# Performance work log

Hardware: AMD Instinct MI355X
Metric: run time of the kernel (lower is better)

The kernel has to match this reference:

```python
import jax, jax.numpy as jnp
import numpy as np

N = 200000      # number of nodes / samples
D = 256         # embedding_dim
K = 20          # n_clusters


def setup_inputs() -> dict:
    key = jax.random.key(0)
    k1, k2 = jax.random.split(key)
    embeddings = jax.random.normal(k1, (N, D), dtype=jnp.float32)
    # indicator P has orthonormal-ish columns in the original (top-k eigenvectors
    # of ZZ^T); random values are fine for a correctness baseline of the math.
    indicator = jax.random.normal(k2, (N, K), dtype=jnp.float32)
    return {"embeddings": embeddings, "indicator": indicator}


def reference(embeddings, indicator):
    # Jc = tr(Z Z^T) - tr(P^T Z Z^T P)
    # tr(Z Z^T) = sum(Z * Z)
    term1 = jnp.sum(embeddings * embeddings)
    # tr(P^T Z Z^T P) = || Z^T P ||_F^2 ; Z^T P is [D, K] (tiny), avoids N x N gram.
    ztp = jnp.einsum('nd,nk->dk', embeddings, indicator)
    term2 = jnp.sum(ztp * ztp)
    return term1 - term2
```

## Files before the change

kernel.cpp:

```cpp
#include <hip/hip_runtime.h>

#define NN 200000
#define DD 256
#define KK 20
#define CHUNK 200
#define NB (NN / CHUNK)
#define RPW (CHUNK / 4)
#define DEPTH 8


typedef __attribute__((address_space(3))) unsigned int lds_uint;
typedef const __attribute__((address_space(1))) unsigned int glb_uint;
#define DMA(gp, lp) \
  __builtin_amdgcn_global_load_lds((glb_uint*)(gp), (lds_uint*)(lp), 16, 0, 0)
#define WAITVM(N) asm volatile("s_waitcnt vmcnt(" #N ")" ::: "memory")

#define SCOMP(i, zv)                                                        \
  {                                                                         \
    const float4* pr_ = (const float4*)(pl + (((i) * 4 + w) * KK));         \
    float4 p0_ = pr_[0], p1_ = pr_[1], p2_ = pr_[2], p3_ = pr_[3],          \
           p4_ = pr_[4];                                                    \
    float zz_[4] = {zv.x, zv.y, zv.z, zv.w};                                \
    float pv_[KK] = {p0_.x, p0_.y, p0_.z, p0_.w, p1_.x, p1_.y, p1_.z,       \
                     p1_.w, p2_.x, p2_.y, p2_.z, p2_.w, p3_.x, p3_.y,       \
                     p3_.z, p3_.w, p4_.x, p4_.y, p4_.z, p4_.w};             \
    t1 += zz_[0] * zz_[0] + zz_[1] * zz_[1];                                \
    t1 += zz_[2] * zz_[2] + zz_[3] * zz_[3];                                \
    _Pragma("unroll") for (int k_ = 0; k_ < KK; ++k_) {                     \
      _Pragma("unroll") for (int c_ = 0; c_ < 4; ++c_)                      \
          acc[k_][c_] += zz_[c_] * pv_[k_];                                 \
    }                                                                       \
  }

#define TAIL(S, N)                                                          \
  {                                                                         \
    WAITVM(N);                                                              \
    float4 z = ((const float4*)(myring + ((S) & (DEPTH - 1)) * DD))[lane];  \
    SCOMP(S, z);                                                            \
  }

__global__ __launch_bounds__(256)
__attribute__((amdgpu_waves_per_eu(3, 3))) void egac_main(
    const float* __restrict__ Z, const float* __restrict__ P,
    float* __restrict__ ztp_part, float* __restrict__ t1_part) {
  __shared__ float ring[4 * DEPTH * DD];
  __shared__ float pl[CHUNK * KK];
  __shared__ float wsum[4];

  const int t = threadIdx.x;
  const int lane = t & 63;
  const int w = t >> 6;
  const int b = blockIdx.x;
  const int base = b * CHUNK;

  {
    const float4* Ps = (const float4*)(P + (size_t)base * KK);
    float4* pd = (float4*)pl;
    for (int i = t; i < CHUNK * KK / 4; i += 256) pd[i] = Ps[i];
  }
  __syncthreads();

  float acc[KK][4];
#pragma unroll
  for (int k = 0; k < KK; ++k)
#pragma unroll
    for (int c = 0; c < 4; ++c) acc[k][c] = 0.f;
  float t1 = 0.f;

  const float* Zblk = Z + (size_t)base * DD;
  float* myring = ring + w * (DEPTH * DD);

#pragma unroll
  for (int q = 0; q < DEPTH; ++q)
    DMA(Zblk + (4 * q + w) * DD + lane * 4, myring + q * DD);

  for (int s = 0; s < RPW - DEPTH; ++s) {
    WAITVM(7);
    float4 z = ((const float4*)(myring + (s & (DEPTH - 1)) * DD))[lane];
    asm volatile("" ::: "memory");
    DMA(Zblk + (4 * (s + DEPTH) + w) * DD + lane * 4,
        myring + (s & (DEPTH - 1)) * DD);
    SCOMP(s, z);
  }
  TAIL(42, 7); TAIL(43, 6); TAIL(44, 5); TAIL(45, 4);
  TAIL(46, 3); TAIL(47, 2); TAIL(48, 1); TAIL(49, 0);

  __syncthreads();
  float(*red)[DD] = (float(*)[DD])ring;
  for (int ph = 0; ph < 4; ++ph) {
    if (w == ph) {
      if (ph == 0) {
#pragma unroll
        for (int k = 0; k < KK; ++k)
          ((float4*)&red[k][0])[lane] =
              make_float4(acc[k][0], acc[k][1], acc[k][2], acc[k][3]);
      } else {
#pragma unroll
        for (int k = 0; k < KK; ++k) {
          float4 r = ((float4*)&red[k][0])[lane];
          r.x += acc[k][0];
          r.y += acc[k][1];
          r.z += acc[k][2];
          r.w += acc[k][3];
          ((float4*)&red[k][0])[lane] = r;
        }
      }
    }
    __syncthreads();
  }

#pragma unroll
  for (int off = 32; off > 0; off >>= 1) t1 += __shfl_xor(t1, off, 64);
  if (lane == 0) wsum[w] = t1;
  __syncthreads();

  float4* dst = (float4*)(ztp_part + (size_t)b * (KK * DD));
  const float4* src = (const float4*)&red[0][0];
#pragma unroll
  for (int i = 0; i < (KK * DD) / (4 * 256); ++i)
    dst[i * 256 + t] = src[i * 256 + t];
  if (t == 0) t1_part[b] = wsum[0] + wsum[1] + wsum[2] + wsum[3];
}

__global__ __launch_bounds__(512) void egac_reduce(
    const float* __restrict__ ztp_part, const float* __restrict__ t1_part,
    float* __restrict__ out, int nb) {
  __shared__ float red[16][32];
  const int t = threadIdx.x;
  const int el = t & 31;
  const int ps = t >> 5;
  const int e = blockIdx.x * 32 + el;

  float s = 0.f;
  for (int p = ps; p < nb; p += 16) s += ztp_part[(size_t)p * (KK * DD) + e];
  red[ps][el] = s;
  __syncthreads();
  for (int sh = 8; sh >= 1; sh >>= 1) {
    if (ps < sh) red[ps][el] += red[ps + sh][el];
    __syncthreads();
  }
  if (t == 0) {
    float ssq = 0.f;
#pragma unroll
    for (int i = 0; i < 32; ++i) {
      float v = red[0][i];
      ssq += v * v;
    }
    atomicAdd(out, -ssq);
  }

  if (blockIdx.x == 0) {
    float v = 0.f;
    for (int i = t; i < nb; i += 512) v += t1_part[i];
#pragma unroll
    for (int off = 32; off > 0; off >>= 1) v += __shfl_xor(v, off, 64);
    __shared__ float w2[8];
    if ((t & 63) == 0) w2[t >> 6] = v;
    __syncthreads();
    if (t == 0) {
      float tt = 0.f;
#pragma unroll
      for (int i = 0; i < 8; ++i) tt += w2[i];
      atomicAdd(out, tt);
    }
  }
}

extern "C" void kernel_launch(void* const* d_in, const int* in_sizes, int n_in,
                              void* d_out, int out_size, void* d_ws,
                              size_t ws_size, hipStream_t stream) {
  const float* Z = (const float*)d_in[0];
  const float* P = (const float*)d_in[1];
  float* out = (float*)d_out;

  float* ztp_part = (float*)d_ws;
  float* t1_part = (float*)d_ws + (size_t)NB * KK * DD;

  hipMemsetAsync(d_out, 0, sizeof(float), stream);
  egac_main<<<NB, 256, 0, stream>>>(Z, P, ztp_part, t1_part);
  egac_reduce<<<160, 512, 0, stream>>>(ztp_part, t1_part, out, NB);
}
```

Baseline: 364.1 us.

## Assign one embedding column per thread and read indicator rows via scalar loads

Changes the work split in the main kernel so each of the 256 threads owns one embedding column across all rows of the chunk, instead of four columns over a quarter of the rows. Indicator rows are now read straight from global memory through wave-uniform (readfirstlane) scalar loads, replacing LDS staging. The 8-deep per-wave ring with explicit vmcnt waits becomes a block-wide double buffer of 20-row tiles synchronised by barriers. This drops the cross-wave LDS reduction at the end and shrinks the accumulator to 20 registers per thread. The cost is a shallower prefetch pipeline and a barrier per stage. There is also a risk that the async LDS DMA is not properly waited on before the barrier.

```diff
diff --git a/kernel.cpp b/kernel.cpp
--- a/kernel.cpp
+++ b/kernel.cpp
@@ -5,47 +5,19 @@
 #define KK 20
 #define CHUNK 200
 #define NB (NN / CHUNK)
-#define RPW (CHUNK / 4)
-#define DEPTH 8
+#define TROWS 20
+#define NSTG (CHUNK / TROWS)
 
 
 typedef __attribute__((address_space(3))) unsigned int lds_uint;
 typedef const __attribute__((address_space(1))) unsigned int glb_uint;
 #define DMA(gp, lp) \
   __builtin_amdgcn_global_load_lds((glb_uint*)(gp), (lds_uint*)(lp), 16, 0, 0)
-#define WAITVM(N) asm volatile("s_waitcnt vmcnt(" #N ")" ::: "memory")
 
-#define SCOMP(i, zv)                                                        \
-  {                                                                         \
-    const float4* pr_ = (const float4*)(pl + (((i) * 4 + w) * KK));         \
-    float4 p0_ = pr_[0], p1_ = pr_[1], p2_ = pr_[2], p3_ = pr_[3],          \
-           p4_ = pr_[4];                                                    \
-    float zz_[4] = {zv.x, zv.y, zv.z, zv.w};                                \
-    float pv_[KK] = {p0_.x, p0_.y, p0_.z, p0_.w, p1_.x, p1_.y, p1_.z,       \
-                     p1_.w, p2_.x, p2_.y, p2_.z, p2_.w, p3_.x, p3_.y,       \
-                     p3_.z, p3_.w, p4_.x, p4_.y, p4_.z, p4_.w};             \
-    t1 += zz_[0] * zz_[0] + zz_[1] * zz_[1];                                \
-    t1 += zz_[2] * zz_[2] + zz_[3] * zz_[3];                                \
-    _Pragma("unroll") for (int k_ = 0; k_ < KK; ++k_) {                     \
-      _Pragma("unroll") for (int c_ = 0; c_ < 4; ++c_)                      \
-          acc[k_][c_] += zz_[c_] * pv_[k_];                                 \
-    }                                                                       \
-  }
-
-#define TAIL(S, N)                                                          \
-  {                                                                         \
-    WAITVM(N);                                                              \
-    float4 z = ((const float4*)(myring + ((S) & (DEPTH - 1)) * DD))[lane];  \
-    SCOMP(S, z);                                                            \
-  }
-
-__global__ __launch_bounds__(256)
-__attribute__((amdgpu_waves_per_eu(3, 3))) void egac_main(
+__global__ __launch_bounds__(256) void egac_main(
     const float* __restrict__ Z, const float* __restrict__ P,
     float* __restrict__ ztp_part, float* __restrict__ t1_part) {
-  __shared__ float ring[4 * DEPTH * DD];
-  __shared__ float pl[CHUNK * KK];
-  __shared__ float wsum[4];
+  __shared__ float ring[2][TROWS * DD];
 
   const int t = threadIdx.x;
   const int lane = t & 63;
@@ -53,72 +25,52 @@
   const int b = blockIdx.x;
   const int base = b * CHUNK;
 
-  {
-    const float4* Ps = (const float4*)(P + (size_t)base * KK);
-    float4* pd = (float4*)pl;
-    for (int i = t; i < CHUNK * KK / 4; i += 256) pd[i] = Ps[i];
+  const float* Zblk = Z + (size_t)base * DD;
+
+  float acc[KK];
+#pragma unroll
+  for (int k = 0; k < KK; ++k) acc[k] = 0.f;
+  float t1 = 0.f;
+
+#pragma unroll
+  for (int q = 0; q < TROWS / 4; ++q) {
+    const int rl = 5 * w + q;
+    DMA(Zblk + rl * DD + lane * 4, &ring[0][rl * DD]);
   }
   __syncthreads();
 
-  float acc[KK][4];
+  for (int s = 0; s < NSTG; ++s) {
+    const int cur = s & 1;
+    if (s + 1 < NSTG) {
 #pragma unroll
-  for (int k = 0; k < KK; ++k)
+      for (int q = 0; q < TROWS / 4; ++q) {
+        const int rl = 5 * w + q;
+        DMA(Zblk + ((s + 1) * TROWS + rl) * DD + lane * 4,
+            &ring[cur ^ 1][rl * DD]);
+      }
+    }
+    const float* zbuf = &ring[cur][0];
 #pragma unroll
-    for (int c = 0; c < 4; ++c) acc[k][c] = 0.f;
-  float t1 = 0.f;
-
-  const float* Zblk = Z + (size_t)base * DD;
-  float* myring = ring + w * (DEPTH * DD);
-
+    for (int i = 0; i < TROWS; ++i) {
+      float z = zbuf[i * DD + t];
+      const int ro = __builtin_amdgcn_readfirstlane((base + s * TROWS + i) * KK);
+      const float* pr = P + ro;
+      t1 += z * z;
 #pragma unroll
-  for (int q = 0; q < DEPTH; ++q)
-    DMA(Zblk + (4 * q + w) * DD + lane * 4, myring + q * DD);
-
-  for (int s = 0; s < RPW - DEPTH; ++s) {
-    WAITVM(7);
-    float4 z = ((const float4*)(myring + (s & (DEPTH - 1)) * DD))[lane];
-    asm volatile("" ::: "memory");
-    DMA(Zblk + (4 * (s + DEPTH) + w) * DD + lane * 4,
-        myring + (s & (DEPTH - 1)) * DD);
-    SCOMP(s, z);
-  }
-  TAIL(42, 7); TAIL(43, 6); TAIL(44, 5); TAIL(45, 4);
-  TAIL(46, 3); TAIL(47, 2); TAIL(48, 1); TAIL(49, 0);
-
-  __syncthreads();
-  float(*red)[DD] = (float(*)[DD])ring;
-  for (int ph = 0; ph < 4; ++ph) {
-    if (w == ph) {
-      if (ph == 0) {
-#pragma unroll
-        for (int k = 0; k < KK; ++k)
-          ((float4*)&red[k][0])[lane] =
-              make_float4(acc[k][0], acc[k][1], acc[k][2], acc[k][3]);
-      } else {
-#pragma unroll
-        for (int k = 0; k < KK; ++k) {
-          float4 r = ((float4*)&red[k][0])[lane];
-          r.x += acc[k][0];
-          r.y += acc[k][1];
-          r.z += acc[k][2];
-          r.w += acc[k][3];
-          ((float4*)&red[k][0])[lane] = r;
-        }
-      }
+      for (int k = 0; k < KK; ++k) acc[k] += z * pr[k];
     }
     __syncthreads();
   }
 
 #pragma unroll
+  for (int k = 0; k < KK; ++k)
+    ztp_part[(size_t)b * (KK * DD) + k * DD + t] = acc[k];
+
+#pragma unroll
   for (int off = 32; off > 0; off >>= 1) t1 += __shfl_xor(t1, off, 64);
+  float* wsum = &ring[0][0];
   if (lane == 0) wsum[w] = t1;
   __syncthreads();
-
-  float4* dst = (float4*)(ztp_part + (size_t)b * (KK * DD));
-  const float4* src = (const float4*)&red[0][0];
-#pragma unroll
-  for (int i = 0; i < (KK * DD) / (4 * 256); ++i)
-    dst[i * 256 + t] = src[i * 256 + t];
   if (t == 0) t1_part[b] = wsum[0] + wsum[1] + wsum[2] + wsum[3];
 }
 
```

After: 325.4 us. -10.6%, faster.
